# Kernel optimization log

Hardware: AMD Instinct MI355X
Metric: run time of the kernel (lower is better)

Reference implementation:

```python
import jax, jax.numpy as jnp
import numpy as np

RADIUS = 3  # local window half-size -> K = (2*RADIUS+1)**2 = 49 taps


def _bilinear_sample_zeros(img_flat, x, y, h, w):
    """Bilinear sampling with zeros padding (grid_sample, align_corners=True).
    img_flat: (B, C, H*W); x, y: (P, K) pixel-space coords. Returns (B, C, P, K).
    align_corners=True denormalization exactly inverts the normalization in the
    original module, so we sample directly at pixel coordinates.
    """
    B, C, _ = img_flat.shape
    x0 = jnp.floor(x)
    y0 = jnp.floor(y)
    out = jnp.zeros((B, C) + x.shape, dtype=img_flat.dtype)
    corners = [
        (x0,       y0,       (x0 + 1 - x) * (y0 + 1 - y)),
        (x0 + 1.0, y0,       (x - x0) * (y0 + 1 - y)),
        (x0,       y0 + 1.0, (x0 + 1 - x) * (y - y0)),
        (x0 + 1.0, y0 + 1.0, (x - x0) * (y - y0)),
    ]
    for xi, yi, wt in corners:
        inb = (xi >= 0) & (xi < w) & (yi >= 0) & (yi < h)
        xi_c = jnp.clip(xi, 0, w - 1).astype(jnp.int32)
        yi_c = jnp.clip(yi, 0, h - 1).astype(jnp.int32)
        idx = (yi_c * w + xi_c).reshape(-1)            # (P*K,)
        v = jnp.take(img_flat, idx, axis=2)            # (B, C, P*K)
        v = v.reshape(B, C, *x.shape)                  # (B, C, P, K)
        out = out + v * (wt * inb.astype(img_flat.dtype))[None, None]
    return out


def reference(feature0, feature1):
    n, c, s, h, w = feature0.shape
    B = n * s
    f0 = feature0.transpose(0, 2, 1, 3, 4).reshape(B, c, h, w)
    f1 = feature1.transpose(0, 2, 1, 3, 4).reshape(B, c, h, w)

    r = RADIUS
    # base pixel coords (x, y), flattened row-major over (h, w) -> (P, 2)
    yy, xx = jnp.meshgrid(jnp.arange(h, dtype=jnp.float32),
                          jnp.arange(w, dtype=jnp.float32), indexing='ij')
    base = jnp.stack([xx, yy], axis=-1).reshape(h * w, 2)  # (P, 2)

    # window offsets (dx, dy), dy outer / dx inner ordering -> (K, 2)
    dys, dxs = jnp.meshgrid(jnp.arange(-r, r + 1, dtype=jnp.float32),
                            jnp.arange(-r, r + 1, dtype=jnp.float32), indexing='ij')
    offs = jnp.stack([dxs, dys], axis=-1).reshape(-1, 2)   # (K, 2)

    sample = base[:, None, :] + offs[None, :, :]           # (P, K, 2)
    valid = ((sample[..., 0] >= 0) & (sample[..., 0] < w) &
             (sample[..., 1] >= 0) & (sample[..., 1] < h))  # (P, K)

    f1_flat = f1.reshape(B, c, h * w)
    wf = _bilinear_sample_zeros(f1_flat, sample[..., 0], sample[..., 1], h, w)  # (B, c, P, K)

    f0_flat = f0.reshape(B, c, h * w)
    corr = jnp.einsum('bcp,bcpk->bpk', f0_flat, wf) / jnp.asarray(c, jnp.float32) ** 0.5
    corr = jnp.where(valid[None], corr, -jnp.inf)
    prob = jax.nn.softmax(corr, axis=-1)                   # (B, P, K)

    corresp = jnp.einsum('bpk,pkj->bpj', prob, sample)     # (B, P, 2) expected (x, y)
    flow = corresp - base[None]                            # (B, P, 2)
    flow = flow.reshape(n, s, h, w, 2).transpose(0, 4, 1, 2, 3)  # (n, 2, s, h, w)
    return flow


def setup_inputs() -> dict:
    key = jax.random.key(0)
    k0, k1 = jax.random.split(key)
    n, c, s, h, w = 2, 64, 4, 64, 44
    feature0 = jax.random.normal(k0, (n, c, s, h, w), dtype=jnp.float32)
    feature1 = jax.random.normal(k1, (n, c, s, h, w), dtype=jnp.float32)
    return {"feature0": feature0, "feature1": feature1}
```

## Files before the change

### kernel.cpp

```cpp
#include <hip/hip_runtime.h>
#include <math.h>

#define N_  2
#define C_  64
#define S_  4
#define H_  64
#define W_  44
#define HW_       (H_ * W_)
#define CH_STRIDE (S_ * HW_)
#define NSTRIDE   (C_ * S_ * HW_)
#define XP  51

typedef _Float16 h2 __attribute__((ext_vector_type(2)));
typedef _Float16 h8 __attribute__((ext_vector_type(8)));

#if defined(__has_builtin)
#  if __has_builtin(__builtin_amdgcn_fdot2)
#    define FDOT2(a, b, c) __builtin_amdgcn_fdot2((a), (b), (c), false)
#  endif
#endif
#ifndef FDOT2
#  define FDOT2(a, b, c) ((float)(a).x * (float)(b).x + (float)(a).y * (float)(b).y + (c))
#endif

__global__ __launch_bounds__(448) void flow_kernel(
    const float* __restrict__ f0,
    const float* __restrict__ f1,
    float* __restrict__ out)
{
    const int lane = threadIdx.x & 63;
    const int wid  = threadIdx.x >> 6;

    const int b = blockIdx.x & 7;
    const int y = blockIdx.x >> 3;
    const int n_idx = b >> 2;
    const int s_idx = b & 3;
    const int base  = n_idx * NSTRIDE + s_idx * HW_;

    __shared__ __align__(16) _Float16 ldsf1[7 * 8 * XP * 8];
    __shared__ float corr[W_][49];

    const int x   = lane;
    const int xe  = min(x, W_ - 1);
    const int row = y + wid - 3;
    const bool row_ok = (row >= 0) && (row < H_);

    float acc[7] = {0.f, 0.f, 0.f, 0.f, 0.f, 0.f, 0.f};

    if (row_ok) {
        const int  xi       = (lane < 44) ? (lane + 3) : ((lane < 47) ? (lane - 44) : lane);
        const bool do_write = (lane <= 50);
        const bool real     = (lane < 44);

        const float* f1p = f1 + base + row * W_ + xe;
        const float* f0p = f0 + base + y   * W_ + xe;

        _Float16* slab = ldsf1 + wid * (8 * XP * 8);

        #pragma unroll 2
        for (int c8 = 0; c8 < 8; ++c8) {
            const float* cp1 = f1p + (size_t)(c8 * 8) * CH_STRIDE;
            const float* cp0 = f0p + (size_t)(c8 * 8) * CH_STRIDE;

            float v[8], a[8];
            #pragma unroll
            for (int j = 0; j < 8; ++j) v[j] = cp1[(size_t)j * CH_STRIDE];
            #pragma unroll
            for (int j = 0; j < 8; ++j) a[j] = cp0[(size_t)j * CH_STRIDE];

            h8 pk;
            #pragma unroll
            for (int j = 0; j < 8; ++j)
                pk[j] = real ? (_Float16)v[j] : (_Float16)0.0f;

            if (do_write)
                *(h8*)&slab[(c8 * XP + xi) * 8] = pk;

            h2 a2[4];
            #pragma unroll
            for (int j = 0; j < 4; ++j) {
                h2 t; t.x = (_Float16)a[2 * j]; t.y = (_Float16)a[2 * j + 1];
                a2[j] = t;
            }

            const _Float16* rp = &slab[(c8 * XP + xe) * 8];
            #pragma unroll
            for (int dx = 0; dx < 7; ++dx) {
                const h8 t = *(const h8*)&rp[dx * 8];
                h2 t01, t23, t45, t67;
                t01.x = t[0]; t01.y = t[1];
                t23.x = t[2]; t23.y = t[3];
                t45.x = t[4]; t45.y = t[5];
                t67.x = t[6]; t67.y = t[7];
                float s = acc[dx];
                s = FDOT2(a2[0], t01, s);
                s = FDOT2(a2[1], t23, s);
                s = FDOT2(a2[2], t45, s);
                s = FDOT2(a2[3], t67, s);
                acc[dx] = s;
            }
        }
    }

    if (x < W_) {
        #pragma unroll
        for (int dx = 0; dx < 7; ++dx)
            corr[x][wid * 7 + dx] = acc[dx] * 0.125f;
    }

    __syncthreads();

    if (wid == 0) {
        float c[49];
        float m = -1e30f;
        #pragma unroll
        for (int k = 0; k < 49; ++k) {
            const int dy  = k / 7, dx = k % 7;
            const int col = x + dx - 3;
            const int rr  = y + dy - 3;
            const bool ok = (col >= 0) && (col < W_) && (rr >= 0) && (rr < H_);
            const float v = ok ? corr[xe][k] : -1e30f;
            c[k] = v;
            m = fmaxf(m, v);
        }
        float S = 0.0f, Sx = 0.0f, Sy = 0.0f;
        #pragma unroll
        for (int k = 0; k < 49; ++k) {
            const float e = __expf(c[k] - m);
            S  += e;
            Sx += e * (float)(k % 7 - 3);
            Sy += e * (float)(k / 7 - 3);
        }
        if (lane < W_) {
            const float inv = 1.0f / S;
            const int ob = (n_idx * 2) * S_ * HW_ + s_idx * HW_ + y * W_ + lane;
            out[ob]            = Sx * inv;
            out[ob + S_ * HW_] = Sy * inv;
        }
    }
}

extern "C" void kernel_launch(void* const* d_in, const int* in_sizes, int n_in,
                              void* d_out, int out_size, void* d_ws, size_t ws_size,
                              hipStream_t stream) {
    const float* f0 = (const float*)d_in[0];
    const float* f1 = (const float*)d_in[1];
    float* out = (float*)d_out;

    flow_kernel<<<8 * H_, 448, 0, stream>>>(f0, f1, out);
}
```

Measured before the change: 68.32 us.

## Drop padded f1 slab, clamp tap indices, and alias corr buffer onto LDS slab

Removes the zero-padded halo columns from the per-wave f16 LDS slab and instead clamps neighbour column indices at read time; invalid taps are masked later in softmax anyway. The f1 staging is split into its own loop ahead of the f0 dot-product loop, and the corr score buffer now reuses the slab memory after an added barrier, shrinking LDS use per block to raise occupancy. Costs an extra __syncthreads and per-tap index clamping, and the staging loop no longer overlaps f1 and f0 loads.

```diff
diff --git a/kernel.cpp b/kernel.cpp
--- a/kernel.cpp
+++ b/kernel.cpp
@@ -9,7 +9,6 @@
 #define HW_       (H_ * W_)
 #define CH_STRIDE (S_ * HW_)
 #define NSTRIDE   (C_ * S_ * HW_)
-#define XP  51
 
 typedef _Float16 h2 __attribute__((ext_vector_type(2)));
 typedef _Float16 h8 __attribute__((ext_vector_type(8)));
@@ -37,8 +36,8 @@
     const int s_idx = b & 3;
     const int base  = n_idx * NSTRIDE + s_idx * HW_;
 
-    __shared__ __align__(16) _Float16 ldsf1[7 * 8 * XP * 8];
-    __shared__ float corr[W_][49];
+    __shared__ __align__(16) char lds_raw[7 * 8 * W_ * 8 * 2];
+    _Float16* lds_h = (_Float16*)lds_raw;
 
     const int x   = lane;
     const int xe  = min(x, W_ - 1);
@@ -47,46 +46,45 @@
 
     float acc[7] = {0.f, 0.f, 0.f, 0.f, 0.f, 0.f, 0.f};
 
+    _Float16* slab = lds_h + wid * (8 * W_ * 8);
+
     if (row_ok) {
-        const int  xi       = (lane < 44) ? (lane + 3) : ((lane < 47) ? (lane - 44) : lane);
-        const bool do_write = (lane <= 50);
-        const bool real     = (lane < 44);
+        const float* f1p = f1 + base + row * W_ + xe;
+        #pragma unroll 2
+        for (int c8 = 0; c8 < 8; ++c8) {
+            const float* cp1 = f1p + (size_t)(c8 * 8) * CH_STRIDE;
+            float v[8];
+            #pragma unroll
+            for (int j = 0; j < 8; ++j) v[j] = cp1[(size_t)j * CH_STRIDE];
+            h8 pk;
+            #pragma unroll
+            for (int j = 0; j < 8; ++j) pk[j] = (_Float16)v[j];
+            if (x < W_)
+                *(h8*)&slab[(c8 * W_ + x) * 8] = pk;
+        }
 
-        const float* f1p = f1 + base + row * W_ + xe;
-        const float* f0p = f0 + base + y   * W_ + xe;
-
-        _Float16* slab = ldsf1 + wid * (8 * XP * 8);
+        const float* f0p = f0 + base + y * W_ + xe;
+        int xt[7];
+        #pragma unroll
+        for (int dx = 0; dx < 7; ++dx)
+            xt[dx] = min(max(x + dx - 3, 0), W_ - 1);
 
         #pragma unroll 2
         for (int c8 = 0; c8 < 8; ++c8) {
-            const float* cp1 = f1p + (size_t)(c8 * 8) * CH_STRIDE;
             const float* cp0 = f0p + (size_t)(c8 * 8) * CH_STRIDE;
-
-            float v[8], a[8];
-            #pragma unroll
-            for (int j = 0; j < 8; ++j) v[j] = cp1[(size_t)j * CH_STRIDE];
+            float a[8];
             #pragma unroll
             for (int j = 0; j < 8; ++j) a[j] = cp0[(size_t)j * CH_STRIDE];
-
-            h8 pk;
-            #pragma unroll
-            for (int j = 0; j < 8; ++j)
-                pk[j] = real ? (_Float16)v[j] : (_Float16)0.0f;
-
-            if (do_write)
-                *(h8*)&slab[(c8 * XP + xi) * 8] = pk;
-
             h2 a2[4];
             #pragma unroll
             for (int j = 0; j < 4; ++j) {
                 h2 t; t.x = (_Float16)a[2 * j]; t.y = (_Float16)a[2 * j + 1];
                 a2[j] = t;
             }
-
-            const _Float16* rp = &slab[(c8 * XP + xe) * 8];
+            const _Float16* rp = &slab[c8 * W_ * 8];
             #pragma unroll
             for (int dx = 0; dx < 7; ++dx) {
-                const h8 t = *(const h8*)&rp[dx * 8];
+                const h8 t = *(const h8*)&rp[xt[dx] * 8];
                 h2 t01, t23, t45, t67;
                 t01.x = t[0]; t01.y = t[1];
                 t23.x = t[2]; t23.y = t[3];
@@ -102,6 +100,9 @@
         }
     }
 
+    __syncthreads();
+
+    float (*corr)[49] = (float(*)[49])lds_raw;
     if (x < W_) {
         #pragma unroll
         for (int dx = 0; dx < 7; ++dx)
```

Measured after the change: 67.30 us. About the same (-1.5%).
